# Optimization experiments

Measured on AMD Instinct MI355X. Metric: run time of the kernel, lower is better.

The kernel has to match this reference:

```python
import jax, jax.numpy as jnp
import numpy as np

B, P, S, D, L = 8, 64, 512, 512, 64


def setup_inputs() -> dict:
    key = jax.random.key(0)
    ks = jax.random.split(key, 12)
    span_repr = jax.random.normal(ks[0], (B, S, D), dtype=jnp.float32)
    predicates = jax.random.randint(ks[1], (B, P), 0, S, dtype=jnp.int64)
    labels = jax.random.randint(ks[2], (B, P, S), 0, L, dtype=jnp.int64)
    long_mask = jnp.ones((B, P, S), dtype=jnp.int64)
    sc = 1.0 / np.sqrt(D)
    # last-layer weights of FFNN linear_p / linear_a (only last layer matters in source)
    Wp = jax.random.normal(ks[3], (D, D), dtype=jnp.float32) * sc
    bp = jnp.zeros((D,), dtype=jnp.float32)
    Wa = jax.random.normal(ks[4], (D, D), dtype=jnp.float32) * sc
    ba = jnp.zeros((D,), dtype=jnp.float32)
    wp = jax.random.normal(ks[5], (D,), dtype=jnp.float32) * sc  # W_p (Linear D->1, no bias)
    wa = jax.random.normal(ks[6], (D,), dtype=jnp.float32) * sc  # W_a
    W1 = jax.random.normal(ks[7], (L, D, D), dtype=jnp.float32) * sc
    W2 = jax.random.normal(ks[8], (2 * D, L), dtype=jnp.float32) * sc
    b = jax.random.normal(ks[9], (1, L), dtype=jnp.float32) * 0.02
    return {"span_repr": span_repr, "predicates": predicates, "labels": labels,
            "long_mask": long_mask, "Wp": Wp, "bp": bp, "Wa": Wa, "ba": ba,
            "wp": wp, "wa": wa, "W1": W1, "W2": W2, "b": b}


def reference(span_repr, predicates, labels, long_mask, Wp, bp, Wa, ba, wp, wa, W1, W2, b):
    d = span_repr.shape[-1]
    # gather predicate representations: [B, P, D]
    pred_repr = jnp.take_along_axis(span_repr, predicates[..., None], axis=1)
    # FFNN (only last layer is effective in source) + scalar projections
    predicates_score = jax.nn.relu(pred_repr @ Wp.T + bp) @ wp        # [B, P]
    argument_score = jax.nn.relu(span_repr @ Wa.T + ba) @ wa          # [B, S]
    p_a_score = predicates_score[:, :, None] + argument_score[:, None, :]  # [B, P, S]
    # biaffine term: matmul(matmul(pred, W1), span^T) -> [B, P, S, L]
    first = jnp.einsum('bpd,lde,bse->bpsl', pred_repr, W1, span_repr)
    # concat(pred, span) @ W2, split to avoid materializing the concat
    second = (jnp.einsum('bpd,dl->bpl', pred_repr, W2[:d])[:, :, None, :]
              + jnp.einsum('bsd,dl->bsl', span_repr, W2[d:])[:, None, :, :])
    combine = first + second + b + p_a_score[..., None]               # [B, P, S, L]
    combine = combine.at[..., -1].set(0.0)
    num_labels = combine.shape[-1]
    # long_mask is all ones, so masked_select is the full flatten
    stack_instance = combine.reshape(-1, num_labels)                  # [B*P*S, L]
    stack_label = labels.reshape(-1)                                  # [B*P*S]
    return stack_instance, stack_label
```

## Files before the change

### kernel.cpp

```cpp
#include <hip/hip_runtime.h>
#include <hip/hip_bf16.h>

typedef __bf16 bf16x8 __attribute__((ext_vector_type(8)));
typedef float f32x4 __attribute__((ext_vector_type(4)));
typedef unsigned short ushort_t;

#define SS 512
#define DD 512
#define LL 64

__device__ __forceinline__ ushort_t f2b(float f) {
    union { float f; unsigned u; } x; x.f = f;
    unsigned r = x.u + 0x7FFFu + ((x.u >> 16) & 1u);
    return (ushort_t)(r >> 16);
}

__device__ __forceinline__ void async16(const void* g, void* l) {
    __builtin_amdgcn_global_load_lds(
        (const __attribute__((address_space(1))) unsigned int*)g,
        (__attribute__((address_space(3))) unsigned int*)l, 16, 0, 0);
}

__device__ __forceinline__ void stage_tile(const ushort_t* __restrict__ A, int lda,
                                           const ushort_t* __restrict__ Bt, int ldb,
                                           int k0, ushort_t* buf) {
    const int t = threadIdx.x;
    const int wbase = (t >> 6) << 10;
#pragma unroll
    for (int p = 0; p < 2; p++) {
        int row = (p << 7) + (t >> 2);
        int kg = (t & 3) ^ ((t >> 3) & 3);
        async16(A + (size_t)row * lda + k0 + kg * 8,
                (char*)buf + (p << 13) + wbase);
        async16(Bt + (size_t)row * ldb + k0 + kg * 8,
                (char*)(buf + 8192) + (p << 13) + wbase);
    }
}

__device__ __forceinline__ void gemm256(const ushort_t* __restrict__ A, int lda,
                                        const ushort_t* __restrict__ Bt, int ldb,
                                        ushort_t* lds, f32x4 (&acc)[8][4]) {
    const int t = threadIdx.x;
    const int lane = t & 63, wid = t >> 6;
    const int wm = wid >> 2, wn = wid & 3;
    const int r15 = lane & 15, kg = lane >> 4;
    const int sx = ((kg ^ ((r15 >> 1) & 3)) << 4);
    const f32x4 z4 = {0.f, 0.f, 0.f, 0.f};
#pragma unroll
    for (int i = 0; i < 8; i++)
#pragma unroll
        for (int j = 0; j < 4; j++) acc[i][j] = z4;

    stage_tile(A, lda, Bt, ldb, 0, lds);
    stage_tile(A, lda, Bt, ldb, 32, lds + 16384);

    for (int T = 0; T < 16; ++T) {
        if (T < 15) asm volatile("s_waitcnt vmcnt(4)" ::: "memory");
        else        asm volatile("s_waitcnt vmcnt(0)" ::: "memory");
        __builtin_amdgcn_s_barrier();
        __builtin_amdgcn_sched_barrier(0);
        const ushort_t* bufA = lds + (T % 3) * 16384;
        const ushort_t* bufB = bufA + 8192;
        const char* pa = (const char*)bufA + (wm * 128 + r15) * 64 + sx;
        const char* pb = (const char*)bufB + (wn * 64 + r15) * 64 + sx;
        bf16x8 af[8], bf[4];
#pragma unroll
        for (int mf = 0; mf < 8; mf++) af[mf] = *(const bf16x8*)(pa + mf * 1024);
#pragma unroll
        for (int nf = 0; nf < 4; nf++) bf[nf] = *(const bf16x8*)(pb + nf * 1024);
        if (T + 2 < 16)
            stage_tile(A, lda, Bt, ldb, (T + 2) * 32, lds + ((T + 2) % 3) * 16384);
#pragma unroll
        for (int mf = 0; mf < 8; mf++)
#pragma unroll
            for (int nf = 0; nf < 4; nf++)
                acc[mf][nf] = __builtin_amdgcn_mfma_f32_16x16x32_bf16(
                    af[mf], bf[nf], acc[mf][nf], 0, 0, 0);
    }
    __syncthreads();
}

__global__ void __launch_bounds__(512, 2) k_U256(const ushort_t* __restrict__ predB,
    const ushort_t* __restrict__ W1T, ushort_t* __restrict__ UB) {
    extern __shared__ ushort_t lds[];
    f32x4 acc[8][4];
    int swz = (blockIdx.x & 7) * 32 + (blockIdx.x >> 3);
    int m0 = (swz & 1) * 256, n0 = (swz >> 1) * 256;
    gemm256(predB + (size_t)m0 * DD, DD, W1T + (size_t)n0 * DD, DD, lds, acc);
    const int t = threadIdx.x, lane = t & 63, wid = t >> 6;
    const int wm = wid >> 2, wn = wid & 3, r15 = lane & 15, kg = lane >> 4;
    ushort_t* my = lds + wid * 4096;
    int gm = m0 + wm * 128, gn = n0 + wn * 64;
#pragma unroll
    for (int ch = 0; ch < 2; ch++) {
#pragma unroll
        for (int mf2 = 0; mf2 < 4; mf2++)
#pragma unroll
            for (int nf = 0; nf < 4; nf++)
#pragma unroll
                for (int j = 0; j < 4; j++)
                    my[(mf2 * 16 + kg * 4 + j) * 64 + nf * 16 + r15] =
                        f2b(acc[ch * 4 + mf2][nf][j]);
#pragma unroll
        for (int it = 0; it < 8; it++) {
            int lr = it * 8 + (lane >> 3);
            bf16x8 v = *(const bf16x8*)(my + lr * 64 + (lane & 7) * 8);
            *(bf16x8*)(UB + (size_t)(gm + ch * 64 + lr) * 32768 + gn + (lane & 7) * 8) = v;
        }
    }
}

__global__ void __launch_bounds__(512, 2) k_out256(const ushort_t* __restrict__ spanB,
    const ushort_t* __restrict__ UB, const float* __restrict__ spanW2,
    const float* __restrict__ predW2, const float* __restrict__ ascore,
    const float* __restrict__ pscore, const float* __restrict__ bias,
    float* __restrict__ out) {
    extern __shared__ ushort_t lds[];
    f32x4 acc[8][4];
    int swz = (blockIdx.x & 7) * 32 + (blockIdx.x >> 3);
    int b = swz >> 5, r = swz & 31;
    int m0 = (r & 1) * 256, n0 = (r >> 1) * 256;
    gemm256(spanB + ((size_t)b * SS + m0) * DD, DD,
            UB + ((size_t)b * 4096 + n0) * DD, DD, lds, acc);
    const int t = threadIdx.x, lane = t & 63, wid = t >> 6;
    const int wm = wid >> 2, wn = wid & 3, r15 = lane & 15, kg = lane >> 4;
    float cn[4]; int nn[4];
#pragma unroll
    for (int nf = 0; nf < 4; nf++) {
        int n = n0 + wn * 64 + nf * 16 + r15;
        nn[nf] = n;
        cn[nf] = bias[n & 63] + predW2[b * 4096 + n] + pscore[b * 64 + (n >> 6)];
    }
#pragma unroll
    for (int mf = 0; mf < 8; mf++)
#pragma unroll
        for (int j = 0; j < 4; j++) {
            int s = m0 + wm * 128 + mf * 16 + kg * 4 + j;
            float as_ = ascore[b * SS + s];
            const float* sw = spanW2 + ((size_t)b * SS + s) * LL;
#pragma unroll
            for (int nf = 0; nf < 4; nf++) {
                int n = nn[nf], l = n & 63, p = n >> 6;
                float v = acc[mf][nf][j] + cn[nf] + as_ + sw[l];
                if (l == LL - 1) v = 0.f;
                out[(((size_t)b * 64 + p) * SS + s) * LL + l] = v;
            }
        }
}

template<int NF>
__device__ __forceinline__ void gemm_core_sb(const ushort_t* __restrict__ A, int lda,
                                             const ushort_t* __restrict__ Bt, int ldb,
                                             int K, ushort_t* As, ushort_t* Bs,
                                             f32x4 (&acc)[4][NF]) {
    constexpr int NBLD = (NF == 4) ? 2 : 1;
    const int tid = threadIdx.x;
    const int lane = tid & 63, wid = tid >> 6;
    const int wr = (wid >> 1) * 64, wc = (wid & 1) * (NF * 16);
    const int r15 = lane & 15, kg = lane >> 4;
    const int o0 = wid * 1024 + lane * 16;
    for (int k0 = 0; k0 < K; k0 += 32) {
#pragma unroll
        for (int p = 0; p < 2; p++) {
            int o = o0 + p * 4096;
            async16(A + (size_t)(o >> 6) * lda + k0 + ((o & 63) >> 1), (char*)As + o);
        }
#pragma unroll
        for (int p = 0; p < NBLD; p++) {
            int o = o0 + p * 4096;
            async16(Bt + (size_t)(o >> 6) * ldb + k0 + ((o & 63) >> 1), (char*)Bs + o);
        }
        __syncthreads();
        bf16x8 af[4], bf[NF];
#pragma unroll
        for (int mf = 0; mf < 4; mf++)
            af[mf] = *(const bf16x8*)(As + (wr + mf * 16 + r15) * 32 + kg * 8);
#pragma unroll
        for (int nf = 0; nf < NF; nf++)
            bf[nf] = *(const bf16x8*)(Bs + (wc + nf * 16 + r15) * 32 + kg * 8);
#pragma unroll
        for (int mf = 0; mf < 4; mf++)
#pragma unroll
            for (int nf = 0; nf < NF; nf++)
                acc[mf][nf] = __builtin_amdgcn_mfma_f32_16x16x32_bf16(
                    af[mf], bf[nf], acc[mf][nf], 0, 0, 0);
        __syncthreads();
    }
}

__global__ __launch_bounds__(256) void k_prep(
    const float* __restrict__ span, const int* __restrict__ preds,
    const int* __restrict__ labels, const float* __restrict__ Wa,
    const float* __restrict__ Wp, const float* __restrict__ W2,
    ushort_t* spanB, ushort_t* predB, ushort_t* WaB, ushort_t* WpB,
    ushort_t* W2aT, ushort_t* W2bT, float* out, float* scores) {
    int blk = blockIdx.x;
    if (blk < 4096) {
        int id = blk * 256 + threadIdx.x;
        if (id < 524288) {
            float4 v = ((const float4*)span)[id];
            ((ushort4*)spanB)[id] = make_ushort4(f2b(v.x), f2b(v.y), f2b(v.z), f2b(v.w));
        } else if (id < 589824) {
            int j = id - 524288;
            int row = j >> 7, c4 = j & 127;
            int b = row >> 6;
            int idx = preds[row];
            float4 v = ((const float4*)(span + ((size_t)(b * SS + idx)) * DD))[c4];
            ((ushort4*)(predB + (size_t)row * DD))[c4] =
                make_ushort4(f2b(v.x), f2b(v.y), f2b(v.z), f2b(v.w));
        } else if (id < 851968) {
            int k = id - 589824;
            out[16777216 + k] = (float)labels[k];
        } else if (id < 917504) {
            int j = id - 851968;
            float4 v = ((const float4*)Wa)[j];
            ((ushort4*)WaB)[j] = make_ushort4(f2b(v.x), f2b(v.y), f2b(v.z), f2b(v.w));
        } else if (id < 983040) {
            int j = id - 917504;
            float4 v = ((const float4*)Wp)[j];
            ((ushort4*)WpB)[j] = make_ushort4(f2b(v.x), f2b(v.y), f2b(v.z), f2b(v.w));
        } else if (id < 1015808) {
            int j = id - 983040;
            W2aT[j] = f2b(W2[(size_t)(j & 511) * LL + (j >> 9)]);
        } else {
            int j = id - 1015808;
            W2bT[j] = f2b(W2[(size_t)((j & 511) + DD) * LL + (j >> 9)]);
        }
    } else {
        int idx = (blk - 4096) * 256 + threadIdx.x;
        if (idx < 4608) scores[idx] = 0.f;
    }
}

__global__ __launch_bounds__(256) void k_small_t(
    const ushort_t* __restrict__ spanB, const ushort_t* __restrict__ predB,
    const ushort_t* __restrict__ WaB, const ushort_t* __restrict__ WpB,
    const ushort_t* __restrict__ W2bT, const ushort_t* __restrict__ W2aT,
    const float* __restrict__ ba_, const float* __restrict__ bp_,
    const float* __restrict__ wa, const float* __restrict__ wp,
    float* ascore, float* pscore, float* spanW2, float* predW2,
    const float* __restrict__ W1, ushort_t* __restrict__ W1T) {
    __shared__ char smem[16640];
    const f32x4 z4 = {0.f, 0.f, 0.f, 0.f};
    int blk = blockIdx.x;
    int lane = threadIdx.x & 63, wid = threadIdx.x >> 6;
    int r15 = lane & 15, kg = lane >> 4;
    if (blk < 144) {
        ushort_t* As = (ushort_t*)smem; ushort_t* Bs = As + 4096;
        const ushort_t *A, *Bt; const float *bias, *w; float* sc; int m0, n0;
        if (blk < 128) { A = spanB; Bt = WaB; bias = ba_; w = wa; sc = ascore;
                         m0 = (blk >> 2) * 128; n0 = (blk & 3) * 128; }
        else { int q = blk - 128; A = predB; Bt = WpB; bias = bp_; w = wp; sc = pscore;
               m0 = (q >> 2) * 128; n0 = (q & 3) * 128; }
        f32x4 acc[4][4];
#pragma unroll
        for (int i = 0; i < 4; i++)
#pragma unroll
            for (int j = 0; j < 4; j++) acc[i][j] = z4;
        gemm_core_sb<4>(A + (size_t)m0 * DD, DD, Bt + (size_t)n0 * DD, DD, DD, As, Bs, acc);
        int wr = (wid >> 1) * 64, wc = (wid & 1) * 64;
#pragma unroll
        for (int mf = 0; mf < 4; mf++)
#pragma unroll
            for (int j = 0; j < 4; j++) {
                float v = 0.f;
#pragma unroll
                for (int nf = 0; nf < 4; nf++) {
                    int col = n0 + wc + nf * 16 + r15;
                    float c = acc[mf][nf][j] + bias[col];
                    if (c > 0.f) v += c * w[col];
                }
                v += __shfl_xor(v, 1); v += __shfl_xor(v, 2);
                v += __shfl_xor(v, 4); v += __shfl_xor(v, 8);
                if (r15 == 0) atomicAdd(&sc[m0 + wr + mf * 16 + kg * 4 + j], v);
            }
    } else if (blk < 180) {
        ushort_t* As = (ushort_t*)smem; ushort_t* Bs = As + 4096;
        int q = blk - 144;
        const ushort_t *A, *Bt; float* C; int m0;
        if (q < 32) { A = spanB; Bt = W2bT; C = spanW2; m0 = q * 128; }
        else { A = predB; Bt = W2aT; C = predW2; m0 = (q - 32) * 128; }
        f32x4 acc[4][2];
#pragma unroll
        for (int i = 0; i < 4; i++) { acc[i][0] = z4; acc[i][1] = z4; }
        gemm_core_sb<2>(A + (size_t)m0 * DD, DD, Bt, DD, DD, As, Bs, acc);
        int wr = (wid >> 1) * 64, wc = (wid & 1) * 32;
#pragma unroll
        for (int mf = 0; mf < 4; mf++)
#pragma unroll
            for (int nf = 0; nf < 2; nf++)
#pragma unroll
                for (int j = 0; j < 4; j++) {
                    int m = m0 + wr + mf * 16 + kg * 4 + j;
                    int n = wc + nf * 16 + r15;
                    C[(size_t)m * LL + n] = acc[mf][nf][j];
                }
    } else {
        float (*tile)[65] = (float(*)[65])smem;
        int q = blk - 180;
        int l = q >> 6, dt = (q & 7) * 64, et = ((q >> 3) & 7) * 64;
        int t = threadIdx.x;
        const float* src = W1 + ((size_t)l * DD + dt) * DD + et;
#pragma unroll
        for (int i = 0; i < 16; i++) {
            int dr = (t >> 6) + i * 4, ec = t & 63;
            tile[dr][ec] = src[(size_t)dr * DD + ec];
        }
        __syncthreads();
        ushort_t* dst = W1T + ((size_t)l * DD + et) * DD + dt;
#pragma unroll
        for (int i = 0; i < 2; i++) {
            int er = (t >> 3) + i * 32, d8 = (t & 7) * 8;
            ushort_t tmp[8];
#pragma unroll
            for (int k = 0; k < 8; k++) tmp[k] = f2b(tile[d8 + k][er]);
            *(uint4*)(dst + (size_t)er * DD + d8) = *(const uint4*)tmp;
        }
    }
}

extern "C" void kernel_launch(void* const* d_in, const int* in_sizes, int n_in,
                              void* d_out, int out_size, void* d_ws, size_t ws_size,
                              hipStream_t stream) {
    const float* span   = (const float*)d_in[0];
    const int*   preds  = (const int*)d_in[1];
    const int*   labels = (const int*)d_in[2];
    const float* Wp     = (const float*)d_in[4];
    const float* bp_    = (const float*)d_in[5];
    const float* Wa     = (const float*)d_in[6];
    const float* ba_    = (const float*)d_in[7];
    const float* wp     = (const float*)d_in[8];
    const float* wa     = (const float*)d_in[9];
    const float* W1     = (const float*)d_in[10];
    const float* W2     = (const float*)d_in[11];
    const float* bias   = (const float*)d_in[12];
    float* out = (float*)d_out;
    char* ws = (char*)d_ws;

    ushort_t* spanB  = (ushort_t*)(ws + 0);
    ushort_t* predB  = (ushort_t*)(ws + 4194304);
    ushort_t* WaB    = (ushort_t*)(ws + 4718592);
    ushort_t* WpB    = (ushort_t*)(ws + 5242880);
    ushort_t* W2aT   = (ushort_t*)(ws + 5767168);
    ushort_t* W2bT   = (ushort_t*)(ws + 5832704);
    ushort_t* W1T    = (ushort_t*)(ws + 5898240);
    ushort_t* UB     = (ushort_t*)(ws + 39452672);
    float*    ascore = (float*)(ws + 73007104);
    float*    pscore = (float*)(ws + 73023488);
    float*    spanW2 = (float*)(ws + 73025536);
    float*    predW2 = (float*)(ws + 74074112);

    hipFuncSetAttribute((const void*)k_U256,
                        hipFuncAttributeMaxDynamicSharedMemorySize, 98304);
    hipFuncSetAttribute((const void*)k_out256,
                        hipFuncAttributeMaxDynamicSharedMemorySize, 98304);

    k_prep<<<4114, 256, 0, stream>>>(span, preds, labels, Wa, Wp, W2,
                                     spanB, predB, WaB, WpB, W2aT, W2bT,
                                     out, ascore);

    k_small_t<<<4276, 256, 0, stream>>>(spanB, predB, WaB, WpB, W2bT, W2aT,
                                        ba_, bp_, wa, wp, ascore, pscore,
                                        spanW2, predW2, W1, W1T);

    k_U256<<<256, 512, 98304, stream>>>(predB, W1T, UB);

    k_out256<<<256, 512, 98304, stream>>>(spanB, UB, spanW2, predW2,
                                          ascore, pscore, bias, out);
}
```

Measured before the change: 89.97 us.

## Fuse W1 fp32-to-bf16 transpose into U GEMM by loading fp32 B directly

Drops the separate pass that transposed and converted W1 (64x512x512 fp32) into a bf16 workspace. The U GEMM now reads fp32 W1 straight from global memory into registers in its natural layout, converts to bf16 in registers, and stages only the A operand through LDS. This avoids writing and re-reading about 33 MB of bf16 workspace, and lets the small-GEMM launch shrink to 180 blocks. In exchange, the B loads are strided scalar fp32 loads (per-lane column reads across rows), which may coalesce poorly and add register pressure in the main GEMM.

```diff
diff --git a/kernel.cpp b/kernel.cpp
--- a/kernel.cpp
+++ b/kernel.cpp
@@ -80,13 +80,81 @@
     __syncthreads();
 }
 
+__device__ __forceinline__ void stageA(const ushort_t* __restrict__ A,
+                                       int k0, ushort_t* buf) {
+    const int t = threadIdx.x;
+    const int wbase = (t >> 6) << 10;
+#pragma unroll
+    for (int p = 0; p < 2; p++) {
+        int row = (p << 7) + (t >> 2);
+        int kg = (t & 3) ^ ((t >> 3) & 3);
+        async16(A + (size_t)row * DD + k0 + kg * 8, (char*)buf + (p << 13) + wbase);
+    }
+}
+
+__device__ __forceinline__ void gemm256_w1(const ushort_t* __restrict__ predB,
+                                           const float* __restrict__ W1le,
+                                           ushort_t* lds, f32x4 (&acc)[8][4]) {
+    const int t = threadIdx.x;
+    const int lane = t & 63, wid = t >> 6;
+    const int wm = wid >> 2, wn = wid & 3;
+    const int r15 = lane & 15, kg = lane >> 4;
+    const int sx = ((kg ^ ((r15 >> 1) & 3)) << 4);
+    const f32x4 z4 = {0.f, 0.f, 0.f, 0.f};
+#pragma unroll
+    for (int i = 0; i < 8; i++)
+#pragma unroll
+        for (int j = 0; j < 4; j++) acc[i][j] = z4;
+
+    const float* bbase = W1le + (size_t)(kg * 8) * DD + wn * 64 + r15;
+    float fb[4][8];
+    auto loadB = [&](int k0) {
+#pragma unroll
+        for (int nf = 0; nf < 4; nf++)
+#pragma unroll
+            for (int j = 0; j < 8; j++)
+                fb[nf][j] = bbase[(size_t)(k0 + j) * DD + nf * 16];
+    };
+
+    stageA(predB, 0, lds);
+    loadB(0);
+    stageA(predB, 32, lds + 8192);
+
+    for (int T = 0; T < 16; ++T) {
+        if (T < 15) asm volatile("s_waitcnt vmcnt(2)" ::: "memory");
+        else        asm volatile("s_waitcnt vmcnt(0)" ::: "memory");
+        __builtin_amdgcn_s_barrier();
+        __builtin_amdgcn_sched_barrier(0);
+        bf16x8 bf[4];
+#pragma unroll
+        for (int nf = 0; nf < 4; nf++)
+#pragma unroll
+            for (int j = 0; j < 8; j++) bf[nf][j] = (__bf16)fb[nf][j];
+        if (T + 1 < 16) loadB((T + 1) * 32);
+        if (T + 2 < 16) stageA(predB, (T + 2) * 32, lds + ((T + 2) % 3) * 8192);
+        const char* pa = (const char*)(lds + (T % 3) * 8192)
+                         + (wm * 128 + r15) * 64 + sx;
+        bf16x8 af[8];
+#pragma unroll
+        for (int mf = 0; mf < 8; mf++) af[mf] = *(const bf16x8*)(pa + mf * 1024);
+#pragma unroll
+        for (int mf = 0; mf < 8; mf++)
+#pragma unroll
+            for (int nf = 0; nf < 4; nf++)
+                acc[mf][nf] = __builtin_amdgcn_mfma_f32_16x16x32_bf16(
+                    af[mf], bf[nf], acc[mf][nf], 0, 0, 0);
+    }
+    __syncthreads();
+}
+
 __global__ void __launch_bounds__(512, 2) k_U256(const ushort_t* __restrict__ predB,
-    const ushort_t* __restrict__ W1T, ushort_t* __restrict__ UB) {
+    const float* __restrict__ W1, ushort_t* __restrict__ UB) {
     extern __shared__ ushort_t lds[];
     f32x4 acc[8][4];
     int swz = (blockIdx.x & 7) * 32 + (blockIdx.x >> 3);
     int m0 = (swz & 1) * 256, n0 = (swz >> 1) * 256;
-    gemm256(predB + (size_t)m0 * DD, DD, W1T + (size_t)n0 * DD, DD, lds, acc);
+    int l = n0 >> 9, e0 = n0 & 511;
+    gemm256_w1(predB + (size_t)m0 * DD, W1 + ((size_t)l * DD) * DD + e0, lds, acc);
     const int t = threadIdx.x, lane = t & 63, wid = t >> 6;
     const int wm = wid >> 2, wn = wid & 3, r15 = lane & 15, kg = lane >> 4;
     ushort_t* my = lds + wid * 4096;
@@ -232,21 +300,19 @@
     }
 }
 
-__global__ __launch_bounds__(256) void k_small_t(
+__global__ __launch_bounds__(256) void k_small(
     const ushort_t* __restrict__ spanB, const ushort_t* __restrict__ predB,
     const ushort_t* __restrict__ WaB, const ushort_t* __restrict__ WpB,
     const ushort_t* __restrict__ W2bT, const ushort_t* __restrict__ W2aT,
     const float* __restrict__ ba_, const float* __restrict__ bp_,
     const float* __restrict__ wa, const float* __restrict__ wp,
-    float* ascore, float* pscore, float* spanW2, float* predW2,
-    const float* __restrict__ W1, ushort_t* __restrict__ W1T) {
-    __shared__ char smem[16640];
+    float* ascore, float* pscore, float* spanW2, float* predW2) {
+    __shared__ ushort_t As[128 * 32], Bs[128 * 32];
     const f32x4 z4 = {0.f, 0.f, 0.f, 0.f};
     int blk = blockIdx.x;
     int lane = threadIdx.x & 63, wid = threadIdx.x >> 6;
     int r15 = lane & 15, kg = lane >> 4;
     if (blk < 144) {
-        ushort_t* As = (ushort_t*)smem; ushort_t* Bs = As + 4096;
         const ushort_t *A, *Bt; const float *bias, *w; float* sc; int m0, n0;
         if (blk < 128) { A = spanB; Bt = WaB; bias = ba_; w = wa; sc = ascore;
                          m0 = (blk >> 2) * 128; n0 = (blk & 3) * 128; }
@@ -274,8 +340,7 @@
                 v += __shfl_xor(v, 4); v += __shfl_xor(v, 8);
                 if (r15 == 0) atomicAdd(&sc[m0 + wr + mf * 16 + kg * 4 + j], v);
             }
-    } else if (blk < 180) {
-        ushort_t* As = (ushort_t*)smem; ushort_t* Bs = As + 4096;
+    } else {
         int q = blk - 144;
         const ushort_t *A, *Bt; float* C; int m0;
         if (q < 32) { A = spanB; Bt = W2bT; C = spanW2; m0 = q * 128; }
@@ -295,27 +360,6 @@
                     int n = wc + nf * 16 + r15;
                     C[(size_t)m * LL + n] = acc[mf][nf][j];
                 }
-    } else {
-        float (*tile)[65] = (float(*)[65])smem;
-        int q = blk - 180;
-        int l = q >> 6, dt = (q & 7) * 64, et = ((q >> 3) & 7) * 64;
-        int t = threadIdx.x;
-        const float* src = W1 + ((size_t)l * DD + dt) * DD + et;
-#pragma unroll
-        for (int i = 0; i < 16; i++) {
-            int dr = (t >> 6) + i * 4, ec = t & 63;
-            tile[dr][ec] = src[(size_t)dr * DD + ec];
-        }
-        __syncthreads();
-        ushort_t* dst = W1T + ((size_t)l * DD + et) * DD + dt;
-#pragma unroll
-        for (int i = 0; i < 2; i++) {
-            int er = (t >> 3) + i * 32, d8 = (t & 7) * 8;
-            ushort_t tmp[8];
-#pragma unroll
-            for (int k = 0; k < 8; k++) tmp[k] = f2b(tile[d8 + k][er]);
-            *(uint4*)(dst + (size_t)er * DD + d8) = *(const uint4*)tmp;
-        }
     }
 }
 
@@ -343,7 +387,6 @@
     ushort_t* WpB    = (ushort_t*)(ws + 5242880);
     ushort_t* W2aT   = (ushort_t*)(ws + 5767168);
     ushort_t* W2bT   = (ushort_t*)(ws + 5832704);
-    ushort_t* W1T    = (ushort_t*)(ws + 5898240);
     ushort_t* UB     = (ushort_t*)(ws + 39452672);
     float*    ascore = (float*)(ws + 73007104);
     float*    pscore = (float*)(ws + 73023488);
@@ -351,7 +394,7 @@
     float*    predW2 = (float*)(ws + 74074112);
 
     hipFuncSetAttribute((const void*)k_U256,
-                        hipFuncAttributeMaxDynamicSharedMemorySize, 98304);
+                        hipFuncAttributeMaxDynamicSharedMemorySize, 65536);
     hipFuncSetAttribute((const void*)k_out256,
                         hipFuncAttributeMaxDynamicSharedMemorySize, 98304);
 
@@ -359,11 +402,11 @@
                                      spanB, predB, WaB, WpB, W2aT, W2bT,
                                      out, ascore);
 
-    k_small_t<<<4276, 256, 0, stream>>>(spanB, predB, WaB, WpB, W2bT, W2aT,
-                                        ba_, bp_, wa, wp, ascore, pscore,
-                                        spanW2, predW2, W1, W1T);
-
-    k_U256<<<256, 512, 98304, stream>>>(predB, W1T, UB);
+    k_small<<<180, 256, 0, stream>>>(spanB, predB, WaB, WpB, W2bT, W2aT,
+                                     ba_, bp_, wa, wp, ascore, pscore,
+                                     spanW2, predW2);
+
+    k_U256<<<256, 512, 65536, stream>>>(predB, W1, UB);
 
     k_out256<<<256, 512, 98304, stream>>>(spanB, UB, spanW2, predW2,
                                           ascore, pscore, bias, out);
```

Result: faster. 87.80 us (-2.4%).
